# Kernel tuning notes

Hardware: AMD Instinct MI355X
Metric: run time of the kernel (lower is better)

## Reference

```python
import jax, jax.numpy as jnp
import numpy as np

N_NODES = 50000
N_EDGES = 1600000
N_GRAPHS = 128
EDGE_DIM = 43
IN_DIM = 35
H = 128          # hidden_dim_1 = hidden_dim_2 = hidden_dim_3
G1, G2 = 64, 32  # gate MLP dims
H6, H7, H8 = 256, 128, 64
U0, U1 = 64, 64  # u_shape


def _linear_params(key, out_dim, in_dim):
    k1, k2 = jax.random.split(key)
    bound = 1.0 / np.sqrt(in_dim)
    W = jax.random.uniform(k1, (out_dim, in_dim), minval=-bound, maxval=bound, dtype=jnp.float32)
    b = jax.random.uniform(k2, (out_dim,), minval=-bound, maxval=bound, dtype=jnp.float32)
    return W, b


def setup_inputs() -> dict:
    key = jax.random.key(0)
    ks = jax.random.split(key, 24)
    x = jax.random.normal(ks[0], (N_NODES, IN_DIM), dtype=jnp.float32)
    edge_index = jax.random.randint(ks[1], (2, N_EDGES), 0, N_NODES, dtype=jnp.int64)
    edge_attr = jax.random.normal(ks[2], (N_EDGES, EDGE_DIM), dtype=jnp.float32)
    batch = jnp.sort(jax.random.randint(ks[3], (N_NODES,), 0, N_GRAPHS, dtype=jnp.int64))
    batch = batch.at[0].set(0).at[-1].set(N_GRAPHS - 1)
    u_soap = jax.random.normal(ks[4], (N_GRAPHS, U0), dtype=jnp.float32)
    u_dimer = jax.random.normal(ks[5], (N_GRAPHS, U1), dtype=jnp.float32)

    W1n, b1n = _linear_params(ks[6], H, IN_DIM + EDGE_DIM)
    W1r, b1r = _linear_params(ks[7], H, IN_DIM)
    W2n, b2n = _linear_params(ks[8], H, H + EDGE_DIM)
    W2r, b2r = _linear_params(ks[9], H, H)
    W3n, b3n = _linear_params(ks[10], H, H + EDGE_DIM)
    W3r, b3r = _linear_params(ks[11], H, H)
    Wg1, bg1 = _linear_params(ks[12], G1, H)
    Wg2, bg2 = _linear_params(ks[13], G2, G1)
    Wg3, bg3 = _linear_params(ks[14], 1, G2)
    Wl1, bl1 = _linear_params(ks[15], H6, U0 + U1 + H)
    Wl2, bl2 = _linear_params(ks[16], H7, H6)
    Wl3, bl3 = _linear_params(ks[17], H8, H7)
    Wl, bl = _linear_params(ks[18], 4, H8)

    return dict(x=x, edge_attr=edge_attr, u_soap=u_soap, u_dimer=u_dimer,
                W1n=W1n, b1n=b1n, W1r=W1r, b1r=b1r,
                W2n=W2n, b2n=b2n, W2r=W2r, b2r=b2r,
                W3n=W3n, b3n=b3n, W3r=W3r, b3r=b3r,
                Wg1=Wg1, bg1=bg1, Wg2=Wg2, bg2=bg2, Wg3=Wg3, bg3=bg3,
                Wl1=Wl1, bl1=bl1, Wl2=Wl2, bl2=bl2, Wl3=Wl3, bl3=bl3,
                Wl=Wl, bl=bl,
                edge_index=edge_index, batch=batch)


def _conv(x, src, edge_attr, Wn, bn, Wr, br):
    # gather source nodes, concat edge features, linear + tanh, scatter-add back to SOURCE (as in original)
    x_adj = jnp.tanh(jnp.concatenate([x[src], edge_attr], axis=1) @ Wn.T + bn)  # [E, H]
    neg_sum = jax.ops.segment_sum(x_adj, src, num_segments=N_NODES)             # [N, H]
    return jnp.tanh(x @ Wr.T + br) + neg_sum


def _segment_softmax(gate, batch, num_segments):
    m = jax.ops.segment_max(gate[:, 0], batch, num_segments=num_segments)
    g = jnp.exp(gate[:, 0] - m[batch])
    s = jax.ops.segment_sum(g, batch, num_segments=num_segments)
    return (g / (s[batch] + 1e-16))[:, None]


def reference(x, edge_attr, u_soap, u_dimer,
              W1n, b1n, W1r, b1r, W2n, b2n, W2r, b2r, W3n, b3n, W3r, b3r,
              Wg1, bg1, Wg2, bg2, Wg3, bg3,
              Wl1, bl1, Wl2, bl2, Wl3, bl3, Wl, bl,
              edge_index, batch):
    src = edge_index[0]
    h = _conv(x, src, edge_attr, W1n, b1n, W1r, b1r)
    h = _conv(h, src, edge_attr, W2n, b2n, W2r, b2r)
    h = _conv(h, src, edge_attr, W3n, b3n, W3r, b3r)

    # GlobalAttention readout
    g = jax.nn.relu(h @ Wg1.T + bg1)
    g = jax.nn.relu(g @ Wg2.T + bg2)
    gate = g @ Wg3.T + bg3                             # [N, 1]
    att = _segment_softmax(gate, batch, N_GRAPHS)      # [N, 1]
    embedding = jax.ops.segment_sum(att * h, batch, num_segments=N_GRAPHS)  # [G, H]

    u = jnp.concatenate([u_soap[:, :U0], u_dimer[:, :U1]], axis=1)
    e2 = jnp.concatenate([embedding, u], axis=1)
    out = jax.nn.relu(e2 @ Wl1.T + bl1)
    out = jax.nn.relu(out @ Wl2.T + bl2)
    out = jax.nn.relu(out @ Wl3.T + bl3)
    out4 = out @ Wl.T + bl                             # [G, 4]
    pred_last = out4.sum(axis=1, keepdims=True)
    return jnp.concatenate([out4, pred_last], axis=1), att
```

## Files before the change

kernel.cpp:

```cpp
#include <hip/hip_runtime.h>
#include <cstdint>
#include <cstddef>

#define N_NODES_C 50000
#define N_EDGES_C 1600000
#define N_GRAPHS_C 128
#define EDGE_DIM_C 43
#define IN_DIM_C 35
#define HDIM_C 128

typedef _Float16 f16x8 __attribute__((ext_vector_type(8)));
typedef float f32x4 __attribute__((ext_vector_type(4)));

__device__ __forceinline__ float fast_tanh(float x) {
    float xc = fminf(9.0f, fmaxf(-9.0f, x));
    float t = __expf(2.0f * xc);
    return (t - 1.0f) * __builtin_amdgcn_rcpf(t + 1.0f);
}


__global__ __launch_bounds__(256) void hist_kernel(const int* __restrict__ src,
                                                   int* __restrict__ cnt) {
    int i = blockIdx.x * 256 + threadIdx.x;
    if (i < N_EDGES_C) atomicAdd(&cnt[src[i]], 1);
}

__global__ __launch_bounds__(1024) void scan_kernel(const int* __restrict__ cnt,
                                                    int* __restrict__ rowptr,
                                                    int* __restrict__ work) {
    __shared__ int wsum[16];
    __shared__ int carry;
    int t = threadIdx.x;
    int lane = t & 63, wid = t >> 6;
    if (t == 0) carry = 0;
    __syncthreads();
    for (int base = 0; base < N_NODES_C; base += 4096) {
        int i0 = base + t * 4;
        int v[4];
        #pragma unroll
        for (int j = 0; j < 4; ++j) {
            int i = i0 + j;
            v[j] = (i < N_NODES_C) ? cnt[i] : 0;
        }
        int pv[4];
        pv[0] = 0;
        #pragma unroll
        for (int j = 1; j < 4; ++j) pv[j] = pv[j-1] + v[j-1];
        int tot = pv[3] + v[3];
        int x = tot;
        #pragma unroll
        for (int off = 1; off < 64; off <<= 1) {
            int xx = __shfl_up(x, off, 64);
            if (lane >= off) x += xx;
        }
        if (lane == 63) wsum[wid] = x;
        __syncthreads();
        if (wid == 0) {
            int wa = (lane < 16) ? wsum[lane] : 0;
            #pragma unroll
            for (int off = 1; off < 16; off <<= 1) {
                int aa = __shfl_up(wa, off, 64);
                if (lane >= off) wa += aa;
            }
            if (lane < 16) wsum[lane] = wa;
        }
        __syncthreads();
        int ex = carry + (wid ? wsum[wid - 1] : 0) + x - tot;
        #pragma unroll
        for (int j = 0; j < 4; ++j) {
            int i = i0 + j;
            if (i < N_NODES_C) {
                int rv = ex + pv[j];
                rowptr[i] = rv; work[i] = rv;
            }
        }
        int totAll = wsum[15];
        __syncthreads();
        if (t == 0) carry += totAll;
        __syncthreads();
    }
    if (t == 0) rowptr[N_NODES_C] = carry;
}

__global__ __launch_bounds__(256) void scatter_kernel(const int* __restrict__ src,
                                                      int* __restrict__ work,
                                                      int* __restrict__ eord) {
    int i = blockIdx.x * 256 + threadIdx.x;
    if (i < N_EDGES_C) {
        int s = src[i];
        int pos = atomicAdd(&work[s], 1);
        eord[pos] = i;
    }
}

__global__ __launch_bounds__(256) void graph_misc(const int* __restrict__ rowptr,
                                                  const int* __restrict__ batch,
                                                  int2* __restrict__ nmeta,
                                                  int* __restrict__ grp) {
    int i = blockIdx.x * 256 + threadIdx.x;
    if (i < N_NODES_C) {
        int rp = rowptr[i];
        int deg = rowptr[i + 1] - rp;
        nmeta[i] = make_int2(deg, rp);
    }
    if (i <= N_GRAPHS_C) {
        int lo = 0, hi = N_NODES_C;
        while (lo < hi) {
            int mid = (lo + hi) >> 1;
            if (batch[mid] < i) lo = mid + 1; else hi = mid;
        }
        grp[i] = lo;
    }
}

__global__ __launch_bounds__(256) void ea2h(const float* __restrict__ EA,
                                            _Float16* __restrict__ EAh) {
    int t = threadIdx.x;
    int e = blockIdx.x * 64 + (t >> 2);
    int q = t & 3;
    if (e >= N_EDGES_C) return;
    const float* pe = EA + (size_t)e * EDGE_DIM_C;
    unsigned int pk[6];
    #pragma unroll
    for (int jj = 0; jj < 6; ++jj) {
        int c0 = q * 12 + 2 * jj;
        float v0 = (c0 < EDGE_DIM_C) ? pe[c0] : 0.0f;
        float v1 = (c0 + 1 < EDGE_DIM_C) ? pe[c0 + 1] : 0.0f;
        unsigned short h0 = __builtin_bit_cast(unsigned short, (_Float16)v0);
        unsigned short h1 = __builtin_bit_cast(unsigned short, (_Float16)v1);
        pk[jj] = (unsigned int)h0 | ((unsigned int)h1 << 16);
    }
    unsigned int* outp = (unsigned int*)(EAh + (size_t)e * 48 + q * 12);
    *(uint2*)(outp)     = make_uint2(pk[0], pk[1]);
    *(uint2*)(outp + 2) = make_uint2(pk[2], pk[3]);
    *(uint2*)(outp + 4) = make_uint2(pk[4], pk[5]);
}


#define BKN 32
__global__ __launch_bounds__(256) void node_gemm(
    const float* __restrict__ A, int K,
    const float* __restrict__ Wn, int ldn, const float* __restrict__ bn,
    const float* __restrict__ Wr, const float* __restrict__ br,
    float* __restrict__ Base, float* __restrict__ Root)
{
    __shared__ float At[BKN][64];
    __shared__ float Bw[BKN][128];
    int t = threadIdx.x;
    int z = blockIdx.y;
    const float* W = z ? Wr : Wn;
    int ldW = z ? K : ldn;
    const float* bias = z ? br : bn;
    float* Out = z ? Root : Base;

    int m0 = blockIdx.x * 64;
    int tn4 = (t % 32) * 4;
    int tm8 = (t / 32) * 8;
    float acc[8][4];
    #pragma unroll
    for (int a = 0; a < 8; a++)
        #pragma unroll
        for (int b = 0; b < 4; b++) acc[a][b] = 0.0f;

    int nkc = (K + BKN - 1) / BKN;
    for (int c = 0; c < nkc; c++) {
        int kc = c * BKN;
        {
            int m_l = t >> 2;
            int q = t & 3;
            int m = m0 + m_l;
            #pragma unroll
            for (int ii = 0; ii < 8; ii++) {
                int kk = q * 8 + ii;
                int k = kc + kk;
                float v = 0.0f;
                if (m < N_NODES_C && k < K) v = A[(size_t)m * K + k];
                At[kk][m_l] = v;
            }
        }
        {
            int j = t % 128;
            int kg2 = t / 128;
            #pragma unroll
            for (int ii = 0; ii < 16; ii++) {
                int kk = kg2 * 16 + ii;
                int k = kc + kk;
                float v = 0.0f;
                if (k < K) v = W[(size_t)j * ldW + k];
                Bw[kk][j] = v;
            }
        }
        __syncthreads();
        #pragma unroll
        for (int kk = 0; kk < BKN; kk++) {
            float a[8], b[4];
            #pragma unroll
            for (int mi = 0; mi < 8; mi++) a[mi] = At[kk][tm8 + mi];
            #pragma unroll
            for (int ni = 0; ni < 4; ni++) b[ni] = Bw[kk][tn4 + ni];
            #pragma unroll
            for (int mi = 0; mi < 8; mi++)
                #pragma unroll
                for (int ni = 0; ni < 4; ni++)
                    acc[mi][ni] = fmaf(a[mi], b[ni], acc[mi][ni]);
        }
        __syncthreads();
    }

    float4 bv = *(const float4*)&bias[tn4];
    #pragma unroll
    for (int mi = 0; mi < 8; mi++) {
        int m = m0 + tm8 + mi;
        if (m < N_NODES_C) {
            float4 o;
            o.x = acc[mi][0] + bv.x;
            o.y = acc[mi][1] + bv.y;
            o.z = acc[mi][2] + bv.z;
            o.w = acc[mi][3] + bv.w;
            if (z) { o.x = fast_tanh(o.x); o.y = fast_tanh(o.y); o.z = fast_tanh(o.z); o.w = fast_tanh(o.w); }
            *(float4*)&Out[(size_t)m * HDIM_C + tn4] = o;
        }
    }
}


__global__ __launch_bounds__(256) void edge_mfma(
    const _Float16* __restrict__ EAh, const int* __restrict__ eord,
    const int2* __restrict__ nmeta,
    const float* __restrict__ Base, const float* __restrict__ Root,
    const float* __restrict__ Wfull, int colOff, int ldW,
    float* __restrict__ Hout)
{
    int t = threadIdx.x;
    int lane = t & 63, wid = t >> 6;
    int l15 = lane & 15, quad = lane >> 4;

    f16x8 bf[8][2];
    #pragma unroll
    for (int nt = 0; nt < 8; ++nt) {
        const float* wr = Wfull + (size_t)(nt * 16 + l15) * ldW + colOff;
        #pragma unroll
        for (int kt = 0; kt < 2; ++kt) {
            f16x8 b;
            #pragma unroll
            for (int j = 0; j < 8; ++j) {
                int k = kt * 32 + quad * 8 + j;
                float v = (k < EDGE_DIM_C) ? wr[k] : 0.0f;
                b[j] = (_Float16)v;
            }
            bf[nt][kt] = b;
        }
    }

    bool useA1 = (quad < 2);
    int off0 = quad * 8;
    int off1 = 32 + ((quad & 1) * 8);

    int nstride = gridDim.x * 4;
    for (int n = blockIdx.x * 4 + wid; n < N_NODES_C; n += nstride) {
        int2 nm = nmeta[n];
        int deg = nm.x, rp = nm.y;
        const float* bp = Base + (size_t)n * HDIM_C;
        float bv[8];
        #pragma unroll
        for (int nt = 0; nt < 8; ++nt) bv[nt] = bp[nt * 16 + l15];
        float cs[8];
        #pragma unroll
        for (int nt = 0; nt < 8; ++nt) cs[nt] = 0.0f;

        int ngr = (deg + 15) >> 4;
        int rbase = quad * 4;
        if (ngr > 0) {
            f16x8 zz8 = {};
            f16x8 a0 = zz8, a1 = zz8;
            if (l15 < deg) {
                int e0 = eord[rp + l15];
                const _Float16* ap = EAh + (size_t)e0 * 48;
                a0 = *(const f16x8*)(ap + off0);
                if (useA1) a1 = *(const f16x8*)(ap + off1);
            }
            for (int gi = 0; gi < ngr; ++gi) {
                f16x8 n0 = zz8, n1 = zz8;
                int rn = (gi + 1) * 16 + l15;
                if (rn < deg) {
                    int en = eord[rp + rn];
                    const _Float16* ap = EAh + (size_t)en * 48;
                    n0 = *(const f16x8*)(ap + off0);
                    if (useA1) n1 = *(const f16x8*)(ap + off1);
                }
                int valid = deg - gi * 16; if (valid > 16) valid = 16;
                f32x4 acc[8];
                #pragma unroll
                for (int nt = 0; nt < 8; ++nt) {
                    f32x4 zz = {0.f, 0.f, 0.f, 0.f};
                    acc[nt] = __builtin_amdgcn_mfma_f32_16x16x32_f16(a0, bf[nt][0], zz, 0, 0, 0);
                    acc[nt] = __builtin_amdgcn_mfma_f32_16x16x32_f16(a1, bf[nt][1], acc[nt], 0, 0, 0);
                }
                #pragma unroll
                for (int nt = 0; nt < 8; ++nt) {
                    #pragma unroll
                    for (int r = 0; r < 4; ++r) {
                        float v = fast_tanh(acc[nt][r] + bv[nt]);
                        cs[nt] += (rbase + r < valid) ? v : 0.0f;
                    }
                }
                a0 = n0; a1 = n1;
            }
        }
        #pragma unroll
        for (int nt = 0; nt < 8; ++nt) {
            cs[nt] += __shfl_xor(cs[nt], 16, 64);
            cs[nt] += __shfl_xor(cs[nt], 32, 64);
        }
        float v0, v1;
        if (quad == 0)      { v0 = cs[0]; v1 = cs[1]; }
        else if (quad == 1) { v0 = cs[2]; v1 = cs[3]; }
        else if (quad == 2) { v0 = cs[4]; v1 = cs[5]; }
        else                { v0 = cs[6]; v1 = cs[7]; }
        int c0 = quad * 32 + l15;
        size_t rowb = (size_t)n * HDIM_C;
        Hout[rowb + c0]      = Root[rowb + c0] + v0;
        Hout[rowb + c0 + 16] = Root[rowb + c0 + 16] + v1;
    }
}


__global__ __launch_bounds__(256) void gate_kernel(
    const float* __restrict__ h,
    const float* __restrict__ Wg1, const float* __restrict__ bg1,
    const float* __restrict__ Wg2, const float* __restrict__ bg2,
    const float* __restrict__ Wg3, const float* __restrict__ bg3,
    float* __restrict__ gate)
{
    __shared__ float Ht[128][65];
    __shared__ float G1[64][65];
    __shared__ float G2[32][65];
    int t = threadIdx.x;
    int m0 = blockIdx.x * 64;
    #pragma unroll
    for (int ii = 0; ii < 32; ++ii) {
        int flat = ii * 256 + t;
        int k = flat & 127, m = flat >> 7;
        float v = (m0 + m < N_NODES_C) ? h[(size_t)(m0 + m) * HDIM_C + k] : 0.0f;
        Ht[k][m] = v;
    }
    __syncthreads();
    int m = t & 63, slab = t >> 6;
    {
        float a[16];
        #pragma unroll
        for (int jj = 0; jj < 16; ++jj) a[jj] = bg1[slab * 16 + jj];
        for (int k = 0; k < 128; ++k) {
            float hv = Ht[k][m];
            #pragma unroll
            for (int jj = 0; jj < 16; ++jj)
                a[jj] = fmaf(Wg1[(size_t)(slab * 16 + jj) * 128 + k], hv, a[jj]);
        }
        #pragma unroll
        for (int jj = 0; jj < 16; ++jj) G1[slab * 16 + jj][m] = fmaxf(a[jj], 0.0f);
    }
    __syncthreads();
    {
        float b[8];
        #pragma unroll
        for (int jj = 0; jj < 8; ++jj) b[jj] = bg2[slab * 8 + jj];
        for (int k = 0; k < 64; ++k) {
            float gv = G1[k][m];
            #pragma unroll
            for (int jj = 0; jj < 8; ++jj)
                b[jj] = fmaf(Wg2[(size_t)(slab * 8 + jj) * 64 + k], gv, b[jj]);
        }
        #pragma unroll
        for (int jj = 0; jj < 8; ++jj) G2[slab * 8 + jj][m] = fmaxf(b[jj], 0.0f);
    }
    __syncthreads();
    if (t < 64 && m0 + t < N_NODES_C) {
        float s = bg3[0];
        #pragma unroll
        for (int k = 0; k < 32; ++k) s = fmaf(Wg3[k], G2[k][t], s);
        gate[m0 + t] = s;
    }
}


__global__ __launch_bounds__(256) void graph_attn(
    const float* __restrict__ gate, const int* __restrict__ grp,
    const float* __restrict__ h3, float* __restrict__ att_out,
    float* __restrict__ emb)
{
    int g = blockIdx.x;
    int t = threadIdx.x;
    int s = grp[g], e = grp[g + 1];
    __shared__ float red[256];
    __shared__ float attb[256];

    float m = -3.4e38f;
    for (int i = s + t; i < e; i += 256) m = fmaxf(m, gate[i]);
    red[t] = m;
    __syncthreads();
    #pragma unroll
    for (int off = 128; off >= 1; off >>= 1) {
        if (t < off) red[t] = fmaxf(red[t], red[t + off]);
        __syncthreads();
    }
    m = red[0];
    __syncthreads();

    float sum = 0.0f;
    for (int i = s + t; i < e; i += 256) sum += __expf(gate[i] - m);
    red[t] = sum;
    __syncthreads();
    #pragma unroll
    for (int off = 128; off >= 1; off >>= 1) {
        if (t < off) red[t] += red[t + off];
        __syncthreads();
    }
    float scale = 1.0f / (red[0] + 1e-16f);
    __syncthreads();

    int j = t & 127;
    int half = t >> 7;
    float acc = 0.0f;
    for (int base = s; base < e; base += 256) {
        int i = base + t;
        float a = 0.0f;
        if (i < e) {
            a = __expf(gate[i] - m) * scale;
            att_out[i] = a;
        }
        attb[t] = a;
        __syncthreads();
        int cnt = e - base; if (cnt > 256) cnt = 256;
        for (int r = half; r < cnt; r += 2)
            acc = fmaf(attb[r], h3[(size_t)(base + r) * HDIM_C + j], acc);
        __syncthreads();
    }
    red[t] = acc;
    __syncthreads();
    if (t < 128) emb[(size_t)g * 128 + t] = red[t] + red[t + 128];
}


__global__ __launch_bounds__(256) void final_mlp(
    const float* __restrict__ emb, const float* __restrict__ us, const float* __restrict__ ud,
    const float* __restrict__ Wl1, const float* __restrict__ bl1,
    const float* __restrict__ Wl2, const float* __restrict__ bl2,
    const float* __restrict__ Wl3, const float* __restrict__ bl3,
    const float* __restrict__ Wl, const float* __restrict__ bl,
    float* __restrict__ out5)
{
    int g = blockIdx.x;
    int t = threadIdx.x;
    __shared__ float e2[256], o1[256], o2[128], o3[64], o4[4];
    if (t < 128) e2[t] = emb[(size_t)g * 128 + t];
    else if (t < 192) e2[t] = us[(size_t)g * 64 + (t - 128)];
    else e2[t] = ud[(size_t)g * 64 + (t - 192)];
    __syncthreads();
    {
        float s = bl1[t];
        const float* wr = Wl1 + (size_t)t * 256;
        #pragma unroll 8
        for (int k = 0; k < 256; k++) s = fmaf(wr[k], e2[k], s);
        o1[t] = fmaxf(s, 0.0f);
    }
    __syncthreads();
    if (t < 128) {
        float s = bl2[t];
        const float* wr = Wl2 + (size_t)t * 256;
        #pragma unroll 8
        for (int k = 0; k < 256; k++) s = fmaf(wr[k], o1[k], s);
        o2[t] = fmaxf(s, 0.0f);
    }
    __syncthreads();
    if (t < 64) {
        float s = bl3[t];
        const float* wr = Wl3 + (size_t)t * 128;
        #pragma unroll 8
        for (int k = 0; k < 128; k++) s = fmaf(wr[k], o2[k], s);
        o3[t] = fmaxf(s, 0.0f);
    }
    __syncthreads();
    if (t < 4) {
        float s = bl[t];
        const float* wr = Wl + (size_t)t * 64;
        #pragma unroll 8
        for (int k = 0; k < 64; k++) s = fmaf(wr[k], o3[k], s);
        o4[t] = s;
    }
    __syncthreads();
    if (t < 5) {
        float v = (t < 4) ? o4[t] : (o4[0] + o4[1] + o4[2] + o4[3]);
        out5[(size_t)g * 5 + t] = v;
    }
}


extern "C" void kernel_launch(void* const* d_in, const int* in_sizes, int n_in,
                              void* d_out, int out_size, void* d_ws, size_t ws_size,
                              hipStream_t stream) {
    const float* x       = (const float*)d_in[0];
    const float* ea      = (const float*)d_in[1];
    const float* u_soap  = (const float*)d_in[2];
    const float* u_dimer = (const float*)d_in[3];
    const float* W1n = (const float*)d_in[4];   const float* b1n = (const float*)d_in[5];
    const float* W1r = (const float*)d_in[6];   const float* b1r = (const float*)d_in[7];
    const float* W2n = (const float*)d_in[8];   const float* b2n = (const float*)d_in[9];
    const float* W2r = (const float*)d_in[10];  const float* b2r = (const float*)d_in[11];
    const float* W3n = (const float*)d_in[12];  const float* b3n = (const float*)d_in[13];
    const float* W3r = (const float*)d_in[14];  const float* b3r = (const float*)d_in[15];
    const float* Wg1 = (const float*)d_in[16];  const float* bg1 = (const float*)d_in[17];
    const float* Wg2 = (const float*)d_in[18];  const float* bg2 = (const float*)d_in[19];
    const float* Wg3 = (const float*)d_in[20];  const float* bg3 = (const float*)d_in[21];
    const float* Wl1 = (const float*)d_in[22];  const float* bl1 = (const float*)d_in[23];
    const float* Wl2 = (const float*)d_in[24];  const float* bl2 = (const float*)d_in[25];
    const float* Wl3 = (const float*)d_in[26];  const float* bl3 = (const float*)d_in[27];
    const float* Wl  = (const float*)d_in[28];  const float* bl  = (const float*)d_in[29];
    const int* eidx  = (const int*)d_in[30];
    const int* batch = (const int*)d_in[31];
    const int* src = eidx;

    float* out5 = (float*)d_out;
    float* att  = out5 + (size_t)N_GRAPHS_C * 5;

    char* p = (char*)d_ws;
    size_t off = 0;
    auto alloc = [&](size_t bytes) -> void* {
        void* r = p + off;
        off += (bytes + 255) & ~(size_t)255;
        return r;
    };
    int* cnt     = (int*)alloc((size_t)N_NODES_C * 4);
    int* rowptr  = (int*)alloc((size_t)(N_NODES_C + 1) * 4);
    int* work    = (int*)alloc((size_t)N_NODES_C * 4);
    int* eord    = (int*)alloc((size_t)(N_EDGES_C + 64) * 4);
    int* grp     = (int*)alloc((size_t)(N_GRAPHS_C + 1) * 4);
    int2* nmeta  = (int2*)alloc((size_t)N_NODES_C * 8);
    float* gate  = (float*)alloc((size_t)N_NODES_C * 4);
    float* emb   = (float*)alloc((size_t)N_GRAPHS_C * 128 * 4);
    float* bufP  = (float*)alloc((size_t)N_NODES_C * HDIM_C * 4);
    float* bufQ  = (float*)alloc((size_t)N_NODES_C * HDIM_C * 4);
    float* bufR  = (float*)alloc((size_t)N_NODES_C * HDIM_C * 4);
    _Float16* EAh = (_Float16*)alloc((size_t)N_EDGES_C * 48 * 2);

    hipMemsetAsync(cnt, 0, (size_t)N_NODES_C * 4, stream);

    int eblocks = (N_EDGES_C + 255) / 256;
    ea2h<<<(N_EDGES_C + 63) / 64, 256, 0, stream>>>(ea, EAh);
    hist_kernel<<<eblocks, 256, 0, stream>>>(src, cnt);
    scan_kernel<<<1, 1024, 0, stream>>>(cnt, rowptr, work);
    scatter_kernel<<<eblocks, 256, 0, stream>>>(src, work, eord);
    graph_misc<<<(N_NODES_C + 255) / 256, 256, 0, stream>>>(rowptr, batch, nmeta, grp);

    dim3 ng((N_NODES_C + 63) / 64, 2);
    int egrid = 2048;

    node_gemm<<<ng, 256, 0, stream>>>(x, IN_DIM_C, W1n, IN_DIM_C + EDGE_DIM_C, b1n, W1r, b1r, bufP, bufQ);
    edge_mfma<<<egrid, 256, 0, stream>>>(EAh, eord, nmeta, bufP, bufQ, W1n, IN_DIM_C, IN_DIM_C + EDGE_DIM_C, bufP);
    node_gemm<<<ng, 256, 0, stream>>>(bufP, HDIM_C, W2n, HDIM_C + EDGE_DIM_C, b2n, W2r, b2r, bufQ, bufR);
    edge_mfma<<<egrid, 256, 0, stream>>>(EAh, eord, nmeta, bufQ, bufR, W2n, HDIM_C, HDIM_C + EDGE_DIM_C, bufQ);
    node_gemm<<<ng, 256, 0, stream>>>(bufQ, HDIM_C, W3n, HDIM_C + EDGE_DIM_C, b3n, W3r, b3r, bufP, bufR);
    edge_mfma<<<egrid, 256, 0, stream>>>(EAh, eord, nmeta, bufP, bufR, W3n, HDIM_C, HDIM_C + EDGE_DIM_C, bufP);

    gate_kernel<<<(N_NODES_C + 63) / 64, 256, 0, stream>>>(bufP, Wg1, bg1, Wg2, bg2, Wg3, bg3, gate);
    graph_attn<<<N_GRAPHS_C, 256, 0, stream>>>(gate, grp, bufP, att, emb);
    final_mlp<<<N_GRAPHS_C, 256, 0, stream>>>(emb, u_soap, u_dimer,
                                              Wl1, bl1, Wl2, bl2, Wl3, bl3, Wl, bl, out5);
}
```

Before: 1.733 ms.

## Prefetch next node's edge tile across nodes and simplify tanh in edge MFMA kernel

The edge MFMA loop now carries a software-pipelined prefetch across node boundaries, so the first edge group of the next node is loaded while the current node's last group is computed. Tanh is reformulated as 1-2/(exp2(k*x)+1), with the scale folded into the bias and applied by an FMA, which drops the clamp and a multiply. Full 16-edge groups also skip the per-row validity masking. The grid shrinks from 2048 to 1280 blocks, giving each wave more nodes to amortise the pipeline, at the cost of less parallelism.

```diff
diff --git a/kernel.cpp b/kernel.cpp
--- a/kernel.cpp
+++ b/kernel.cpp
@@ -16,6 +16,21 @@
     float xc = fminf(9.0f, fmaxf(-9.0f, x));
     float t = __expf(2.0f * xc);
     return (t - 1.0f) * __builtin_amdgcn_rcpf(t + 1.0f);
+}
+
+#define TANH_K 2.8853900817779268f
+
+__device__ __forceinline__ float exp2f_fast(float x) {
+#if __has_builtin(__builtin_amdgcn_exp2f)
+    return __builtin_amdgcn_exp2f(x);
+#else
+    return __expf(x * 0.69314718055994531f);
+#endif
+}
+
+__device__ __forceinline__ float tanh_from_arg(float a) {
+    float t = exp2f_fast(a);
+    return fmaf(-2.0f, __builtin_amdgcn_rcpf(t + 1.0f), 1.0f);
 }
 
 
@@ -255,39 +270,64 @@
     bool useA1 = (quad < 2);
     int off0 = quad * 8;
     int off1 = 32 + ((quad & 1) * 8);
+    int rbase = quad * 4;
 
     int nstride = gridDim.x * 4;
-    for (int n = blockIdx.x * 4 + wid; n < N_NODES_C; n += nstride) {
-        int2 nm = nmeta[n];
+    int n = blockIdx.x * 4 + wid;
+    if (n >= N_NODES_C) return;
+
+    f16x8 zz8 = {};
+    f16x8 a0 = zz8, a1 = zz8;
+    bool pf = false;
+    int2 nm = nmeta[n];
+
+    while (true) {
+        int n2 = n + nstride;
+        bool has2 = (n2 < N_NODES_C);
+        int2 nm2 = make_int2(0, 0);
+        if (has2) nm2 = nmeta[n2];
+
         int deg = nm.x, rp = nm.y;
+        int ngr = (deg + 15) >> 4;
+
         const float* bp = Base + (size_t)n * HDIM_C;
-        float bv[8];
-        #pragma unroll
-        for (int nt = 0; nt < 8; ++nt) bv[nt] = bp[nt * 16 + l15];
+        float b2[8];
+        #pragma unroll
+        for (int nt = 0; nt < 8; ++nt) b2[nt] = TANH_K * bp[nt * 16 + l15];
+
         float cs[8];
         #pragma unroll
         for (int nt = 0; nt < 8; ++nt) cs[nt] = 0.0f;
 
-        int ngr = (deg + 15) >> 4;
-        int rbase = quad * 4;
         if (ngr > 0) {
-            f16x8 zz8 = {};
-            f16x8 a0 = zz8, a1 = zz8;
-            if (l15 < deg) {
-                int e0 = eord[rp + l15];
-                const _Float16* ap = EAh + (size_t)e0 * 48;
-                a0 = *(const f16x8*)(ap + off0);
-                if (useA1) a1 = *(const f16x8*)(ap + off1);
+            if (!pf) {
+                a0 = zz8; a1 = zz8;
+                if (l15 < deg) {
+                    int e0 = eord[rp + l15];
+                    const _Float16* ap = EAh + (size_t)e0 * 48;
+                    a0 = *(const f16x8*)(ap + off0);
+                    if (useA1) a1 = *(const f16x8*)(ap + off1);
+                }
             }
             for (int gi = 0; gi < ngr; ++gi) {
-                f16x8 n0 = zz8, n1 = zz8;
-                int rn = (gi + 1) * 16 + l15;
-                if (rn < deg) {
-                    int en = eord[rp + rn];
-                    const _Float16* ap = EAh + (size_t)en * 48;
-                    n0 = *(const f16x8*)(ap + off0);
-                    if (useA1) n1 = *(const f16x8*)(ap + off1);
+                f16x8 p0 = zz8, p1 = zz8;
+                if (gi + 1 < ngr) {
+                    int rn = (gi + 1) * 16 + l15;
+                    if (rn < deg) {
+                        int en = eord[rp + rn];
+                        const _Float16* ap = EAh + (size_t)en * 48;
+                        p0 = *(const f16x8*)(ap + off0);
+                        if (useA1) p1 = *(const f16x8*)(ap + off1);
+                    }
+                } else if (has2 && nm2.x > 0) {
+                    if (l15 < nm2.x) {
+                        int en = eord[nm2.y + l15];
+                        const _Float16* ap = EAh + (size_t)en * 48;
+                        p0 = *(const f16x8*)(ap + off0);
+                        if (useA1) p1 = *(const f16x8*)(ap + off1);
+                    }
                 }
+
                 int valid = deg - gi * 16; if (valid > 16) valid = 16;
                 f32x4 acc[8];
                 #pragma unroll
@@ -296,17 +336,33 @@
                     acc[nt] = __builtin_amdgcn_mfma_f32_16x16x32_f16(a0, bf[nt][0], zz, 0, 0, 0);
                     acc[nt] = __builtin_amdgcn_mfma_f32_16x16x32_f16(a1, bf[nt][1], acc[nt], 0, 0, 0);
                 }
-                #pragma unroll
-                for (int nt = 0; nt < 8; ++nt) {
+                if (valid == 16) {
                     #pragma unroll
-                    for (int r = 0; r < 4; ++r) {
-                        float v = fast_tanh(acc[nt][r] + bv[nt]);
-                        cs[nt] += (rbase + r < valid) ? v : 0.0f;
+                    for (int nt = 0; nt < 8; ++nt) {
+                        float s = tanh_from_arg(fmaf(TANH_K, acc[nt][0], b2[nt]));
+                        s += tanh_from_arg(fmaf(TANH_K, acc[nt][1], b2[nt]));
+                        s += tanh_from_arg(fmaf(TANH_K, acc[nt][2], b2[nt]));
+                        s += tanh_from_arg(fmaf(TANH_K, acc[nt][3], b2[nt]));
+                        cs[nt] += s;
+                    }
+                } else {
+                    int rq = valid - rbase;
+                    #pragma unroll
+                    for (int nt = 0; nt < 8; ++nt) {
+                        #pragma unroll
+                        for (int r = 0; r < 4; ++r) {
+                            float v = tanh_from_arg(fmaf(TANH_K, acc[nt][r], b2[nt]));
+                            cs[nt] += (r < rq) ? v : 0.0f;
+                        }
                     }
                 }
-                a0 = n0; a1 = n1;
+                a0 = p0; a1 = p1;
             }
-        }
+            pf = has2 && (nm2.x > 0);
+        } else {
+            pf = false;
+        }
+
         #pragma unroll
         for (int nt = 0; nt < 8; ++nt) {
             cs[nt] += __shfl_xor(cs[nt], 16, 64);
@@ -321,6 +377,9 @@
         size_t rowb = (size_t)n * HDIM_C;
         Hout[rowb + c0]      = Root[rowb + c0] + v0;
         Hout[rowb + c0 + 16] = Root[rowb + c0 + 16] + v1;
+
+        if (!has2) break;
+        n = n2; nm = nm2;
     }
 }
 
@@ -552,7 +611,7 @@
     graph_misc<<<(N_NODES_C + 255) / 256, 256, 0, stream>>>(rowptr, batch, nmeta, grp);
 
     dim3 ng((N_NODES_C + 63) / 64, 2);
-    int egrid = 2048;
+    int egrid = 1280;
 
     node_gemm<<<ng, 256, 0, stream>>>(x, IN_DIM_C, W1n, IN_DIM_C + EDGE_DIM_C, b1n, W1r, b1r, bufP, bufQ);
     edge_mfma<<<egrid, 256, 0, stream>>>(EAh, eord, nmeta, bufP, bufQ, W1n, IN_DIM_C, IN_DIM_C + EDGE_DIM_C, bufP);
```

Result: faster. 1.626 ms (-6.2%).
